# Kernel optimization log

Hardware: AMD Instinct MI355X
Metric: run time of the kernel (lower is better)

## Reference

```python
import jax, jax.numpy as jnp
import numpy as np

NUM_CLASSES = 5  # fill_max for graph_label


def setup_inputs() -> dict:
    key = jax.random.key(0)
    k1, k2, k3, k4, k5, k6 = jax.random.split(key, 6)
    z_dim, hid = 64, 256  # hid = 4 * z_dim
    G, N = 16, 40000      # set_length, set_size
    graph_input = jax.random.normal(k1, (G, N, z_dim), dtype=jnp.float32)
    graph_label = jax.random.randint(k2, (N,), 0, NUM_CLASSES)
    # GraphConvolution params, uniform(-stdv, stdv) with stdv = 1/sqrt(out_features)
    s1 = 1.0 / np.sqrt(hid)
    s2 = 1.0 / np.sqrt(z_dim)
    W1 = jax.random.uniform(k3, (z_dim, hid), minval=-s1, maxval=s1, dtype=jnp.float32)
    b1 = jax.random.uniform(k4, (hid,), minval=-s1, maxval=s1, dtype=jnp.float32)
    W2 = jax.random.uniform(k5, (hid, z_dim), minval=-s2, maxval=s2, dtype=jnp.float32)
    b2 = jax.random.uniform(k6, (z_dim,), minval=-s2, maxval=s2, dtype=jnp.float32)
    return {"graph_input": graph_input, "graph_label": graph_label,
            "W1": W1, "b1": b1, "W2": W2, "b2": b2}


def reference(graph_input, graph_label, W1, b1, W2, b2):
    # The label-induced adjacency (same-class clique + self loop, row-normalized)
    # has rows equal to 1/n_c over the node's class, so spmm(adj, x) is the
    # per-class mean of x. Dropout is identity in eval mode.
    dt = graph_input.dtype
    onehot = (graph_label[None, :] == jnp.arange(NUM_CLASSES)[:, None]).astype(dt)  # [C,N]
    counts = jnp.maximum(onehot.sum(axis=1), jnp.asarray(1, dt))                    # [C]

    def gcn(x, W, b):
        support = jnp.einsum('gnd,df->gnf', x, W)                              # dense mm
        cls_mean = jnp.einsum('cn,gnf->gcf', onehot, support) / counts[None, :, None]
        return cls_mean[:, graph_label, :] + b                                 # spmm + bias

    h = jax.nn.relu(gcn(graph_input, W1, b1))
    return graph_input + gcn(h, W2, b2)
```

## Files before the change

### kernel.cpp

```cpp
#include <hip/hip_runtime.h>

#define G 16
#define N 40000
#define D 64
#define HID 256
#define C 5

#define NB 50
#define CHUNKS 800

#define CHUNKO 400
#define NBO (N / CHUNKO)

typedef float v4f __attribute__((ext_vector_type(4)));


__global__ __launch_bounds__(256) void k_sums(const v4f* __restrict__ x,
                                              const int* __restrict__ lab,
                                              v4f* __restrict__ Spart,
                                              float* __restrict__ cntpart) {
    const int g    = blockIdx.y;
    const int b    = blockIdx.x;
    const int base = b * CHUNKS;
    const int tid  = threadIdx.x;
    const int q    = tid & 15;
    const int r    = tid >> 4;

    v4f acc[C];
    float cacc[C];
#pragma unroll
    for (int c = 0; c < C; ++c) { acc[c] = (v4f)0.f; cacc[c] = 0.f; }

    const v4f* xg = x + (size_t)g * N * 16;
#pragma unroll 2
    for (int i = r; i < CHUNKS; i += 16) {
        const int n   = base + i;
        const int lbl = lab[n];
        v4f v = xg[(size_t)n * 16 + q];
#pragma unroll
        for (int c = 0; c < C; ++c) {
            const float m = (lbl == c) ? 1.f : 0.f;
            acc[c] += m * v;
            cacc[c] += m;
        }
    }

    __shared__ v4f   red[C][16][16];
    __shared__ float scnt[C][16];
#pragma unroll
    for (int c = 0; c < C; ++c) {
        red[c][r][q] = acc[c];
        if (q == 0) scnt[c][r] = cacc[c];
    }
    __syncthreads();
    for (int s = 8; s >= 1; s >>= 1) {
        if (r < s) {
#pragma unroll
            for (int c = 0; c < C; ++c) {
                red[c][r][q] += red[c][r + s][q];
                if (q == 0) scnt[c][r] += scnt[c][r + s];
            }
        }
        __syncthreads();
    }
    if (r == 0) {
#pragma unroll
        for (int c = 0; c < C; ++c)
            Spart[(((size_t)g * NB + b) * C + c) * 16 + q] = red[c][0][q];
    }
    if (g == 0 && tid < C)
        cntpart[b * C + tid] = scnt[tid][0];
}

__global__ __launch_bounds__(256) void k_mlp(const float* __restrict__ Spart,
                                             const float* __restrict__ cntpart,
                                             const float* __restrict__ W1,
                                             const float* __restrict__ b1,
                                             const float* __restrict__ W2,
                                             const float* __restrict__ b2,
                                             float* __restrict__ M2) {
    const int gc  = blockIdx.x;
    const int g   = gc / C;
    const int c   = gc % C;
    const int tid = threadIdx.x;
    const int d   = tid & 63;
    const int grp = tid >> 6;

    __shared__ float rs[4][D];
    __shared__ float ccnt;
    __shared__ float xm[D];
    __shared__ float H[HID];

    float s = 0.f;
    for (int b = grp; b < NB; b += 4)
        s += Spart[(((size_t)g * NB + b) * C + c) * D + d];
    rs[grp][d] = s;

    if (tid == 0) ccnt = 0.f;
    __syncthreads();
    if (tid < NB) atomicAdd(&ccnt, cntpart[tid * C + c]);
    __syncthreads();

    if (tid < D) {
        float cc = ccnt;
        if (cc < 1.f) cc = 1.f;
        xm[tid] = (rs[0][tid] + rs[1][tid] + rs[2][tid] + rs[3][tid]) / cc;
    }
    __syncthreads();

    float m1 = 0.f;
#pragma unroll
    for (int dd = 0; dd < D; ++dd) m1 = fmaf(xm[dd], W1[dd * HID + tid], m1);
    m1 += b1[tid];
    H[tid] = m1 > 0.f ? m1 : 0.f;
    __syncthreads();
    if (tid < D) {
        float m2 = 0.f;
        for (int f = 0; f < HID; ++f) m2 = fmaf(H[f], W2[f * D + tid], m2);
        M2[gc * D + tid] = m2 + b2[tid];
    }
}

__global__ __launch_bounds__(256) void k_out(const v4f* __restrict__ x,
                                             const int* __restrict__ lab,
                                             const v4f* __restrict__ M2,
                                             v4f* __restrict__ out) {
    const int g    = blockIdx.y;
    const int base = blockIdx.x * CHUNKO;
    const int tid  = threadIdx.x;
    const int q    = tid & 15;
    const int r    = tid >> 4;

    __shared__ v4f m2s[C][16];
    if (tid < C * 16) m2s[tid >> 4][tid & 15] = M2[(size_t)g * C * 16 + tid];
    __syncthreads();

    const size_t goff = (size_t)g * N * 16;
#pragma unroll 2
    for (int i = r; i < CHUNKO; i += 16) {
        const int n   = base + i;
        const int lbl = lab[n];
        v4f v = x[goff + (size_t)n * 16 + q];
        v += m2s[lbl][q];
        __builtin_nontemporal_store(v, out + goff + (size_t)n * 16 + q);
    }
}

extern "C" void kernel_launch(void* const* d_in, const int* in_sizes, int n_in,
                              void* d_out, int out_size, void* d_ws, size_t ws_size,
                              hipStream_t stream) {
    const float* x   = (const float*)d_in[0];
    const int*   lab = (const int*)d_in[1];
    const float* W1  = (const float*)d_in[2];
    const float* b1  = (const float*)d_in[3];
    const float* W2  = (const float*)d_in[4];
    const float* b2  = (const float*)d_in[5];
    float* out = (float*)d_out;

    float* wsf     = (float*)d_ws;
    float* Spart   = wsf;
    float* cntpart = wsf + 256000;
    float* M2      = wsf + 256256;

    dim3 gs(NB, G);
    k_sums<<<gs, 256, 0, stream>>>((const v4f*)x, lab, (v4f*)Spart, cntpart);

    k_mlp<<<G * C, 256, 0, stream>>>(Spart, cntpart, W1, b1, W2, b2, M2);

    dim3 go(NBO, G);
    k_out<<<go, 256, 0, stream>>>((const v4f*)x, lab, (const v4f*)M2,
                                  (v4f*)out);
}
```

Measured before the change: 329.4 us.

## Give each wavefront a contiguous node range and move class counting into MLP kernel

The sums and output kernels now hand each 64-lane wavefront its own contiguous block of nodes, instead of striding all 256 threads across the whole chunk. The sums kernel's inner loop is also unrolled further, and the per-class count accumulation is dropped from it. Class counts are instead recomputed in the MLP kernel by scanning the labels with a shuffle reduction, and the second matmul there is split across all four wavefronts rather than one. The aim is better memory access locality, more loads in flight, and less ALU work in the bandwidth-bound passes, in exchange for each of the 80 MLP blocks scanning all 40000 labels.

Measured after the change: 338.6 us. 2.8% more time.

```diff
diff --git a/kernel.cpp b/kernel.cpp
--- a/kernel.cpp
+++ b/kernel.cpp
@@ -8,72 +8,67 @@
 
 #define NB 50
 #define CHUNKS 800
+#define WNODES 200
 
 #define CHUNKO 400
 #define NBO (N / CHUNKO)
+#define WNODESO 100
 
 typedef float v4f __attribute__((ext_vector_type(4)));
 
 
 __global__ __launch_bounds__(256) void k_sums(const v4f* __restrict__ x,
                                               const int* __restrict__ lab,
-                                              v4f* __restrict__ Spart,
-                                              float* __restrict__ cntpart) {
+                                              v4f* __restrict__ Spart) {
     const int g    = blockIdx.y;
     const int b    = blockIdx.x;
-    const int base = b * CHUNKS;
     const int tid  = threadIdx.x;
-    const int q    = tid & 15;
-    const int r    = tid >> 4;
+    const int w    = tid >> 6;
+    const int lane = tid & 63;
+    const int q    = lane & 15;
+    const int rr   = lane >> 4;
+    const int base = b * CHUNKS + w * WNODES;
 
     v4f acc[C];
-    float cacc[C];
 #pragma unroll
-    for (int c = 0; c < C; ++c) { acc[c] = (v4f)0.f; cacc[c] = 0.f; }
+    for (int c = 0; c < C; ++c) acc[c] = (v4f)0.f;
 
     const v4f* xg = x + (size_t)g * N * 16;
-#pragma unroll 2
-    for (int i = r; i < CHUNKS; i += 16) {
-        const int n   = base + i;
+#pragma unroll 4
+    for (int it = 0; it < WNODES / 4; ++it) {
+        const int n   = base + it * 4 + rr;
         const int lbl = lab[n];
         v4f v = xg[(size_t)n * 16 + q];
 #pragma unroll
-        for (int c = 0; c < C; ++c) {
-            const float m = (lbl == c) ? 1.f : 0.f;
-            acc[c] += m * v;
-            cacc[c] += m;
-        }
+        for (int c = 0; c < C; ++c)
+            acc[c] += ((lbl == c) ? 1.f : 0.f) * v;
     }
 
-    __shared__ v4f   red[C][16][16];
-    __shared__ float scnt[C][16];
+    __shared__ v4f red[C][16][16];
+    const int row = w * 4 + rr;
 #pragma unroll
-    for (int c = 0; c < C; ++c) {
-        red[c][r][q] = acc[c];
-        if (q == 0) scnt[c][r] = cacc[c];
-    }
+    for (int c = 0; c < C; ++c) red[c][row][q] = acc[c];
     __syncthreads();
+
+    const int qd = tid & 15;
+    const int rd = tid >> 4;
     for (int s = 8; s >= 1; s >>= 1) {
-        if (r < s) {
+        if (rd < s) {
 #pragma unroll
-            for (int c = 0; c < C; ++c) {
-                red[c][r][q] += red[c][r + s][q];
-                if (q == 0) scnt[c][r] += scnt[c][r + s];
-            }
+            for (int c = 0; c < C; ++c)
+                red[c][rd][qd] += red[c][rd + s][qd];
         }
         __syncthreads();
     }
-    if (r == 0) {
+    if (rd == 0) {
 #pragma unroll
         for (int c = 0; c < C; ++c)
-            Spart[(((size_t)g * NB + b) * C + c) * 16 + q] = red[c][0][q];
+            Spart[(((size_t)g * NB + b) * C + c) * 16 + qd] = red[c][0][qd];
     }
-    if (g == 0 && tid < C)
-        cntpart[b * C + tid] = scnt[tid][0];
 }
 
 __global__ __launch_bounds__(256) void k_mlp(const float* __restrict__ Spart,
-                                             const float* __restrict__ cntpart,
+                                             const int* __restrict__ lab,
                                              const float* __restrict__ W1,
                                              const float* __restrict__ b1,
                                              const float* __restrict__ W2,
@@ -87,22 +82,25 @@
     const int grp = tid >> 6;
 
     __shared__ float rs[4][D];
-    __shared__ float ccnt;
     __shared__ float xm[D];
     __shared__ float H[HID];
+    __shared__ float pr[4][D];
+    __shared__ int   wcnt[4];
 
     float s = 0.f;
-    for (int b = grp; b < NB; b += 4)
-        s += Spart[(((size_t)g * NB + b) * C + c) * D + d];
+    for (int bb = grp; bb < NB; bb += 4)
+        s += Spart[(((size_t)g * NB + bb) * C + c) * D + d];
     rs[grp][d] = s;
 
-    if (tid == 0) ccnt = 0.f;
-    __syncthreads();
-    if (tid < NB) atomicAdd(&ccnt, cntpart[tid * C + c]);
+    int cnt = 0;
+    for (int n = tid; n < N; n += 256) cnt += (lab[n] == c) ? 1 : 0;
+#pragma unroll
+    for (int off = 32; off >= 1; off >>= 1) cnt += __shfl_down(cnt, off);
+    if ((tid & 63) == 0) wcnt[tid >> 6] = cnt;
     __syncthreads();
 
     if (tid < D) {
-        float cc = ccnt;
+        float cc = (float)(wcnt[0] + wcnt[1] + wcnt[2] + wcnt[3]);
         if (cc < 1.f) cc = 1.f;
         xm[tid] = (rs[0][tid] + rs[1][tid] + rs[2][tid] + rs[3][tid]) / cc;
     }
@@ -114,11 +112,17 @@
     m1 += b1[tid];
     H[tid] = m1 > 0.f ? m1 : 0.f;
     __syncthreads();
-    if (tid < D) {
-        float m2 = 0.f;
-        for (int f = 0; f < HID; ++f) m2 = fmaf(H[f], W2[f * D + tid], m2);
-        M2[gc * D + tid] = m2 + b2[tid];
-    }
+
+    float p = 0.f;
+    const int f0 = grp * 64;
+#pragma unroll
+    for (int ff = 0; ff < 64; ++ff)
+        p = fmaf(H[f0 + ff], W2[(f0 + ff) * D + d], p);
+    pr[grp][d] = p;
+    __syncthreads();
+    if (tid < D)
+        M2[(size_t)gc * D + tid] =
+            pr[0][tid] + pr[1][tid] + pr[2][tid] + pr[3][tid] + b2[tid];
 }
 
 __global__ __launch_bounds__(256) void k_out(const v4f* __restrict__ x,
@@ -126,19 +130,21 @@
                                              const v4f* __restrict__ M2,
                                              v4f* __restrict__ out) {
     const int g    = blockIdx.y;
-    const int base = blockIdx.x * CHUNKO;
     const int tid  = threadIdx.x;
-    const int q    = tid & 15;
-    const int r    = tid >> 4;
+    const int w    = tid >> 6;
+    const int lane = tid & 63;
+    const int q    = lane & 15;
+    const int rr   = lane >> 4;
+    const int base = blockIdx.x * CHUNKO + w * WNODESO;
 
     __shared__ v4f m2s[C][16];
     if (tid < C * 16) m2s[tid >> 4][tid & 15] = M2[(size_t)g * C * 16 + tid];
     __syncthreads();
 
     const size_t goff = (size_t)g * N * 16;
-#pragma unroll 2
-    for (int i = r; i < CHUNKO; i += 16) {
-        const int n   = base + i;
+#pragma unroll 5
+    for (int it = 0; it < WNODESO / 4; ++it) {
+        const int n   = base + it * 4 + rr;
         const int lbl = lab[n];
         v4f v = x[goff + (size_t)n * 16 + q];
         v += m2s[lbl][q];
@@ -157,15 +163,14 @@
     const float* b2  = (const float*)d_in[5];
     float* out = (float*)d_out;
 
-    float* wsf     = (float*)d_ws;
-    float* Spart   = wsf;
-    float* cntpart = wsf + 256000;
-    float* M2      = wsf + 256256;
+    float* wsf   = (float*)d_ws;
+    float* Spart = wsf;
+    float* M2    = wsf + 256000;
 
     dim3 gs(NB, G);
-    k_sums<<<gs, 256, 0, stream>>>((const v4f*)x, lab, (v4f*)Spart, cntpart);
+    k_sums<<<gs, 256, 0, stream>>>((const v4f*)x, lab, (v4f*)Spart);
 
-    k_mlp<<<G * C, 256, 0, stream>>>(Spart, cntpart, W1, b1, W2, b2, M2);
+    k_mlp<<<G * C, 256, 0, stream>>>(Spart, lab, W1, b1, W2, b2, M2);
 
     dim3 go(NBO, G);
     k_out<<<go, 256, 0, stream>>>((const v4f*)x, lab, (const v4f*)M2,
```
